# Kernel optimization log

Measured on AMD Instinct MI355X. Metric: run time of the kernel, lower is better.

The kernel has to match this reference:

```python
import jax, jax.numpy as jnp
import numpy as np

B = 65536      # total rows = env_batch(8192) * n_slave(8)
DIN = 256      # input_shape
H = 64         # slave_hidden_dim
A = 32         # attention_dim
NACT = 14      # n_actions
NS = 8         # n_slave


def setup_inputs() -> dict:
    key = jax.random.key(0)
    ks = jax.random.split(key, 12)
    s = 0.05
    return {
        "obs": jax.random.normal(ks[0], (B, DIN), jnp.float32),
        "hidden_state": jax.random.normal(ks[1], (B, H), jnp.float32),
        "enc_W": jax.random.normal(ks[2], (DIN, H), jnp.float32) * s,
        "enc_b": jnp.zeros((H,), jnp.float32),
        "gru_Wih": jax.random.normal(ks[3], (3 * H, H), jnp.float32) * s,
        "gru_Whh": jax.random.normal(ks[4], (3 * H, H), jnp.float32) * s,
        "gru_bih": jnp.zeros((3 * H,), jnp.float32),
        "gru_bhh": jnp.zeros((3 * H,), jnp.float32),
        "qW": jax.random.normal(ks[5], (H, A), jnp.float32) * s,
        "kW": jax.random.normal(ks[6], (H, A), jnp.float32) * s,
        "vW": jax.random.normal(ks[7], (H, A), jnp.float32) * s,
        "vb": jnp.zeros((A,), jnp.float32),
        "decW": jax.random.normal(ks[8], (H + A, NACT), jnp.float32) * s,
        "decb": jnp.zeros((NACT,), jnp.float32),
        "n_slave": NS,
    }


def reference(obs, hidden_state, enc_W, enc_b, gru_Wih, gru_Whh, gru_bih, gru_bhh,
              qW, kW, vW, vb, decW, decb, n_slave):
    # encoding + ReLU
    x = jax.nn.relu(obs @ enc_W + enc_b)                      # [B, H]
    # torch GRUCell: r,z,n gate order in weight rows
    gx = x @ gru_Wih.T + gru_bih                              # [B, 3H]
    gh = hidden_state @ gru_Whh.T + gru_bhh                   # [B, 3H]
    xr, xz, xn = jnp.split(gx, 3, axis=-1)
    hr, hz, hn = jnp.split(gh, 3, axis=-1)
    r = jax.nn.sigmoid(xr + hr)
    z = jax.nn.sigmoid(xz + hz)
    n = jnp.tanh(xn + r * hn)
    h_out = (1.0 - z) * n + z * hidden_state                  # [B, H]

    Ad = qW.shape[-1]
    q = (h_out @ qW).reshape(-1, n_slave, Ad)                 # [b, n, A]
    k = (h_out @ kW).reshape(-1, n_slave, Ad)
    v = jax.nn.relu(h_out @ vW + vb).reshape(-1, n_slave, Ad)

    # exclude-self attention == diagonal-masked softmax attention
    scores = jnp.einsum('bia,bja->bij', q, k) / jnp.sqrt(jnp.float32(Ad))
    eye = jnp.eye(n_slave, dtype=bool)
    scores = jnp.where(eye, jnp.float32(-1e9), scores)
    attn = jax.nn.softmax(scores, axis=-1)                    # [b, n, n]
    xatt = jnp.einsum('bij,bja->bia', attn, v).reshape(-1, Ad)  # [B, A]

    out = jnp.concatenate([h_out, xatt], axis=-1) @ decW + decb  # [B, n_actions]
    return (out, h_out)
```

## Files before the change

kernel.cpp:

```cpp
#include <hip/hip_runtime.h>


#define NACT 14
#define BTOT 65536

typedef unsigned int  u32;
typedef unsigned short u16;
using short8 = __attribute__((ext_vector_type(8))) short;
using f32x4  = __attribute__((ext_vector_type(4))) float;

#define ENCB 0
#define WIHB 16896
#define WHHB 30720
#define QKVB 44544
#define DECB 51456
#define WTOT 53120

__device__ u16   g_wbuf[WTOT];
__device__ float g_bias[256];

__device__ __forceinline__ u32 f2bf(float f){
  u32 x = __float_as_uint(f);
  return (x + 0x7fffu + ((x >> 16) & 1u)) >> 16;
}
__device__ __forceinline__ u32 pk2(float a, float b){ return f2bf(a) | (f2bf(b) << 16); }
__device__ __forceinline__ float sigm(float x){ return 1.0f / (1.0f + __expf(-x)); }
__device__ __forceinline__ float tanhp(float x){ return 1.0f - 2.0f / (__expf(2.0f * x) + 1.0f); }
__device__ __forceinline__ short8 as_s8(uint4 v){ union { uint4 u; short8 s; } x; x.u = v; return x.s; }

#define MFMA16(a,b,c) __builtin_amdgcn_mfma_f32_16x16x32_bf16((a),(b),(c),0,0,0)

__global__ void prep(const float* __restrict__ encW, const float* __restrict__ Wih,
                     const float* __restrict__ Whh,  const float* __restrict__ qW,
                     const float* __restrict__ kW,   const float* __restrict__ vW,
                     const float* __restrict__ decW, const float* __restrict__ bih,
                     const float* __restrict__ bhh)
{
  int i = blockIdx.x * 256 + threadIdx.x;
  if (blockIdx.x == 0) {
    int n = threadIdx.x & 63, g = threadIdx.x >> 6;
    float v;
    if      (g == 0) v = bih[n]       + bhh[n];
    else if (g == 1) v = bih[64 + n]  + bhh[64 + n];
    else if (g == 2) v = bih[128 + n];
    else             v = bhh[128 + n];
    g_bias[threadIdx.x] = v;
  }
  if (i >= WTOT) return;
  float val = 0.f;
  if (i < WIHB)      { int n = i / 264, k = i % 264;            if (k < 256) val = encW[k * 64 + n]; }
  else if (i < WHHB) { int j = i - WIHB; int n = j / 72, k = j % 72; if (k < 64) val = Wih[n * 64 + k]; }
  else if (i < QKVB) { int j = i - WHHB; int n = j / 72, k = j % 72; if (k < 64) val = Whh[n * 64 + k]; }
  else if (i < DECB) { int j = i - QKVB; int n = j / 72, k = j % 72;
    if (k < 64) { int m = n >> 5, nn = n & 31;
      val = (m == 0) ? qW[k * 32 + nn] * 0.17677669529663687f
          : (m == 1) ? kW[k * 32 + nn] : vW[k * 32 + nn]; } }
  else { int j = i - DECB; int n = j / 104, k = j % 104; if (n < 14 && k < 96) val = decW[k * 14 + n]; }
  g_wbuf[i] = (u16)f2bf(val);
}

__global__ __launch_bounds__(256, 3)
void commslave_main(const float* __restrict__ obs,  const float* __restrict__ hid,
                    const float* __restrict__ encb, const float* __restrict__ vb,
                    const float* __restrict__ decb, float* __restrict__ out)
{
  __shared__ __align__(16) u16 ldsU[23040];

  const int tid  = threadIdx.x;
  const int lane = tid & 63;
  const int w    = tid >> 6;
  const int quad = lane >> 4;
  const int l16  = lane & 15;
  const int M0   = 16 * w;
  const int gr   = blockIdx.x * 64 + M0;

  float* Sf = (float*)(ldsU + 9216) + w * (16 * 68);
  float* Af = (float*)(ldsU + 9216) + w * (16 * 108);

  f32x4 ce[4];
  #pragma unroll
  for (int t = 0; t < 4; t++) { float bv = encb[16 * t + l16]; ce[t] = (f32x4){bv, bv, bv, bv}; }
  #pragma unroll
  for (int ks = 0; ks < 8; ks++) {
    const float* ap = obs + (size_t)(gr + l16) * 256 + ks * 32 + quad * 8;
    float4 a0 = *(const float4*)ap, a1 = *(const float4*)(ap + 4);
    short8 a = as_s8(make_uint4(pk2(a0.x, a0.y), pk2(a0.z, a0.w), pk2(a1.x, a1.y), pk2(a1.z, a1.w)));
    #pragma unroll
    for (int t = 0; t < 4; t++) {
      short8 b = as_s8(*(const uint4*)&g_wbuf[ENCB + (16 * t + l16) * 264 + ks * 32 + quad * 8]);
      ce[t] = MFMA16(a, b, ce[t]);
    }
  }
  #pragma unroll
  for (int t = 0; t < 4; t++)
    #pragma unroll
    for (int r = 0; r < 4; r++)
      Sf[(quad * 4 + r) * 68 + 16 * t + l16] = fmaxf(ce[t][r], 0.f);
  #pragma unroll
  for (int i = 0; i < 2; i++) {
    int c = lane + 64 * i, lr = c >> 3, j = c & 7;
    const float* sp = &Sf[lr * 68 + 8 * j];
    float4 v0 = *(const float4*)sp, v1 = *(const float4*)(sp + 4);
    *(uint4*)&ldsU[(M0 + lr) * 72 + 8 * j] =
        make_uint4(pk2(v0.x, v0.y), pk2(v0.z, v0.w), pk2(v1.x, v1.y), pk2(v1.z, v1.w));
  }
  __syncthreads();

  short8 ax[2], ah[2];
  #pragma unroll
  for (int ks = 0; ks < 2; ks++) {
    ax[ks] = *(const short8*)&ldsU[(M0 + l16) * 72 + ks * 32 + quad * 8];
    const float* hp = hid + (size_t)(gr + l16) * 64 + ks * 32 + quad * 8;
    float4 h0 = *(const float4*)hp, h1 = *(const float4*)(hp + 4);
    ah[ks] = as_s8(make_uint4(pk2(h0.x, h0.y), pk2(h0.z, h0.w), pk2(h1.x, h1.y), pk2(h1.z, h1.w)));
  }
  #pragma unroll
  for (int u = 0; u < 4; u++) {
    f32x4 g6[6];
    #pragma unroll
    for (int t = 0; t < 6; t++) g6[t] = (f32x4){0.f, 0.f, 0.f, 0.f};
    #pragma unroll
    for (int g = 0; g < 3; g++) {
      int row = 64 * g + 16 * u + l16;
      #pragma unroll
      for (int ks = 0; ks < 2; ks++) {
        short8 bi = as_s8(*(const uint4*)&g_wbuf[WIHB + row * 72 + ks * 32 + quad * 8]);
        g6[g] = MFMA16(ax[ks], bi, g6[g]);
        short8 bh = as_s8(*(const uint4*)&g_wbuf[WHHB + row * 72 + ks * 32 + quad * 8]);
        g6[3 + g] = MFMA16(ah[ks], bh, g6[3 + g]);
      }
    }
    int nc = 16 * u + l16;
    float brz = g_bias[nc], bzz = g_bias[64 + nc], bni = g_bias[128 + nc], bnh = g_bias[192 + nc];
    #pragma unroll
    for (int r = 0; r < 4; r++) {
      float hp = hid[(size_t)(gr + quad * 4 + r) * 64 + nc];
      float rg = sigm(g6[0][r] + g6[3][r] + brz);
      float zg = sigm(g6[1][r] + g6[4][r] + bzz);
      float nn = tanhp(g6[2][r] + bni + rg * (g6[5][r] + bnh));
      Sf[(quad * 4 + r) * 68 + nc] = (1.f - zg) * nn + zg * hp;
    }
  }
  float* outH = out + (size_t)BTOT * NACT;
  #pragma unroll
  for (int i = 0; i < 2; i++) {
    int c = lane + 64 * i, lr = c >> 3, j = c & 7;
    const float* sp = &Sf[lr * 68 + 8 * j];
    float4 v0 = *(const float4*)sp, v1 = *(const float4*)(sp + 4);
    *(uint4*)&ldsU[4608 + (M0 + lr) * 72 + 8 * j] =
        make_uint4(pk2(v0.x, v0.y), pk2(v0.z, v0.w), pk2(v1.x, v1.y), pk2(v1.z, v1.w));
    *(float4*)(outH + (size_t)(gr + lr) * 64 + 8 * j)     = v0;
    *(float4*)(outH + (size_t)(gr + lr) * 64 + 8 * j + 4) = v1;
  }
  __syncthreads();

  short8 hx[2];
  #pragma unroll
  for (int ks = 0; ks < 2; ks++)
    hx[ks] = *(const short8*)&ldsU[4608 + (M0 + l16) * 72 + ks * 32 + quad * 8];
  f32x4 cq[6];
  #pragma unroll
  for (int t = 0; t < 6; t++) {
    float bv = (t >= 4) ? vb[16 * (t - 4) + l16] : 0.f;
    cq[t] = (f32x4){bv, bv, bv, bv};
  }
  #pragma unroll
  for (int ks = 0; ks < 2; ks++)
    #pragma unroll
    for (int t = 0; t < 6; t++) {
      short8 b = as_s8(*(const uint4*)&g_wbuf[QKVB + (16 * t + l16) * 72 + ks * 32 + quad * 8]);
      cq[t] = MFMA16(hx[ks], b, cq[t]);
    }
  #pragma unroll
  for (int t = 0; t < 6; t++)
    #pragma unroll
    for (int r = 0; r < 4; r++) {
      float v = cq[t][r];
      if (t >= 4) v = fmaxf(v, 0.f);
      Af[(quad * 4 + r) * 108 + 16 * t + l16] = v;
    }

  {
    const int r_l = lane >> 2, s4 = lane & 3;
    const int gb = r_l & 8, ri = r_l & 7;
    const float* fq = &Af[r_l * 108];
    float sc[2];
    #pragma unroll
    for (int jj = 0; jj < 2; jj++) {
      int j = s4 + 4 * jj;
      const float* fk = &Af[(gb + j) * 108 + 32];
      float d = 0.f;
      #pragma unroll
      for (int a4 = 0; a4 < 32; a4 += 4) {
        float4 q4 = *(const float4*)&fq[a4];
        float4 k4 = *(const float4*)&fk[a4];
        d += q4.x * k4.x + q4.y * k4.y + q4.z * k4.z + q4.w * k4.w;
      }
      sc[jj] = (j == ri) ? -1e30f : d;
    }
    float m = fmaxf(sc[0], sc[1]);
    m = fmaxf(m, __shfl_xor(m, 1));
    m = fmaxf(m, __shfl_xor(m, 2));
    float p0 = (s4     == ri) ? 0.f : __expf(sc[0] - m);
    float p1 = (s4 + 4 == ri) ? 0.f : __expf(sc[1] - m);
    float sum = p0 + p1;
    sum += __shfl_xor(sum, 1);
    sum += __shfl_xor(sum, 2);
    float inv = 1.f / sum;
    Af[r_l * 108 + 96 + s4]  = p0 * inv;
    Af[r_l * 108 + 100 + s4] = p1 * inv;
    float xa[8] = {0, 0, 0, 0, 0, 0, 0, 0};
    #pragma unroll
    for (int j = 0; j < 8; j++) {
      float aj = Af[r_l * 108 + 96 + j];
      const float* fv = &Af[(gb + j) * 108 + 64 + 8 * s4];
      float4 w0 = *(const float4*)fv, w1 = *(const float4*)(fv + 4);
      xa[0] += aj * w0.x; xa[1] += aj * w0.y; xa[2] += aj * w0.z; xa[3] += aj * w0.w;
      xa[4] += aj * w1.x; xa[5] += aj * w1.y; xa[6] += aj * w1.z; xa[7] += aj * w1.w;
    }
    *(uint4*)&ldsU[(M0 + r_l) * 72 + 8 * s4] =
        make_uint4(pk2(xa[0], xa[1]), pk2(xa[2], xa[3]), pk2(xa[4], xa[5]), pk2(xa[6], xa[7]));
  }
  __syncthreads();

  {
    float db = (l16 < NACT) ? decb[l16] : 0.f;
    f32x4 co = (f32x4){db, db, db, db};
    #pragma unroll
    for (int ks = 0; ks < 2; ks++) {
      short8 a = *(const short8*)&ldsU[4608 + (M0 + l16) * 72 + ks * 32 + quad * 8];
      short8 b = as_s8(*(const uint4*)&g_wbuf[DECB + l16 * 104 + ks * 32 + quad * 8]);
      co = MFMA16(a, b, co);
    }
    short8 a2 = *(const short8*)&ldsU[(M0 + l16) * 72 + quad * 8];
    short8 b2 = as_s8(*(const uint4*)&g_wbuf[DECB + l16 * 104 + 64 + quad * 8]);
    co = MFMA16(a2, b2, co);
    if (l16 < NACT) {
      #pragma unroll
      for (int r = 0; r < 4; r++)
        out[(size_t)(gr + quad * 4 + r) * NACT + l16] = co[r];
    }
  }
}

extern "C" void kernel_launch(void* const* d_in, const int* in_sizes, int n_in,
                              void* d_out, int out_size, void* d_ws, size_t ws_size,
                              hipStream_t stream) {
  (void)in_sizes; (void)n_in; (void)d_ws; (void)ws_size; (void)out_size;
  const float* obs  = (const float*)d_in[0];
  const float* hid  = (const float*)d_in[1];
  const float* encW = (const float*)d_in[2];
  const float* encb = (const float*)d_in[3];
  const float* Wih  = (const float*)d_in[4];
  const float* Whh  = (const float*)d_in[5];
  const float* bih  = (const float*)d_in[6];
  const float* bhh  = (const float*)d_in[7];
  const float* qW   = (const float*)d_in[8];
  const float* kW   = (const float*)d_in[9];
  const float* vW   = (const float*)d_in[10];
  const float* vb   = (const float*)d_in[11];
  const float* decW = (const float*)d_in[12];
  const float* decb = (const float*)d_in[13];
  float* out = (float*)d_out;

  prep<<<(WTOT + 255) / 256, 256, 0, stream>>>(encW, Wih, Whh, qW, kW, vW, decW, bih, bhh);
  commslave_main<<<BTOT / 64, 256, 0, stream>>>(obs, hid, encb, vb, decb, out);
}
```

Measured before the change: 163.3 us.

## Shrink blocks, stage hidden state in LDS as bf16, use hardware bf16 pack

Blocks drop from 256 to 128 threads and LDS from 46KB to about 18KB to raise occupancy. The hidden state is loaded once with coalesced reads, stored in LDS as bf16, and reused for the GRU MFMA operand and the blend term instead of being read from global memory twice. V is kept in bf16 LDS and the f32 attention buffer is merged with the scratch area. h_out is written to global memory at the end from its bf16 copy, and float-to-bf16 packing now uses the v_cvt_pk_bf16_f32 instruction. The cost is lower precision: the hidden-state blend term and the h_out output are now rounded to bf16.

```diff
diff --git a/kernel.cpp b/kernel.cpp
--- a/kernel.cpp
+++ b/kernel.cpp
@@ -19,11 +19,17 @@
 __device__ u16   g_wbuf[WTOT];
 __device__ float g_bias[256];
 
-__device__ __forceinline__ u32 f2bf(float f){
+__device__ __forceinline__ u32 f2bf_rne(float f){
   u32 x = __float_as_uint(f);
   return (x + 0x7fffu + ((x >> 16) & 1u)) >> 16;
 }
-__device__ __forceinline__ u32 pk2(float a, float b){ return f2bf(a) | (f2bf(b) << 16); }
+__device__ __forceinline__ u32 pk2(float a, float b){
+  u32 d;
+  asm("v_cvt_pk_bf16_f32 %0, %1, %2" : "=v"(d) : "v"(a), "v"(b));
+  return d;
+}
+__device__ __forceinline__ float blo(u32 u){ return __uint_as_float(u << 16); }
+__device__ __forceinline__ float bhi(u32 u){ return __uint_as_float(u & 0xffff0000u); }
 __device__ __forceinline__ float sigm(float x){ return 1.0f / (1.0f + __expf(-x)); }
 __device__ __forceinline__ float tanhp(float x){ return 1.0f - 2.0f / (__expf(2.0f * x) + 1.0f); }
 __device__ __forceinline__ short8 as_s8(uint4 v){ union { uint4 u; short8 s; } x; x.u = v; return x.s; }
@@ -56,15 +62,15 @@
       val = (m == 0) ? qW[k * 32 + nn] * 0.17677669529663687f
           : (m == 1) ? kW[k * 32 + nn] : vW[k * 32 + nn]; } }
   else { int j = i - DECB; int n = j / 104, k = j % 104; if (n < 14 && k < 96) val = decW[k * 14 + n]; }
-  g_wbuf[i] = (u16)f2bf(val);
-}
-
-__global__ __launch_bounds__(256, 3)
+  g_wbuf[i] = (u16)f2bf_rne(val);
+}
+
+__global__ __launch_bounds__(128, 4)
 void commslave_main(const float* __restrict__ obs,  const float* __restrict__ hid,
                     const float* __restrict__ encb, const float* __restrict__ vb,
                     const float* __restrict__ decb, float* __restrict__ out)
 {
-  __shared__ __align__(16) u16 ldsU[23040];
+  __shared__ __align__(16) u16 ldsU[8960];
 
   const int tid  = threadIdx.x;
   const int lane = tid & 63;
@@ -72,10 +78,16 @@
   const int quad = lane >> 4;
   const int l16  = lane & 15;
   const int M0   = 16 * w;
-  const int gr   = blockIdx.x * 64 + M0;
-
-  float* Sf = (float*)(ldsU + 9216) + w * (16 * 68);
-  float* Af = (float*)(ldsU + 9216) + w * (16 * 108);
+  const int gr   = blockIdx.x * 32 + M0;
+  float* Sf = (float*)(ldsU + 4608) + w * (16 * 68);
+
+  #pragma unroll
+  for (int i = 0; i < 4; i++) {
+    int c = lane + 64 * i;
+    int lr = c >> 4, c4 = c & 15;
+    float4 v = ((const float4*)hid)[(size_t)(gr + lr) * 16 + c4];
+    *(uint2*)&ldsU[2304 + (M0 + lr) * 72 + c4 * 4] = make_uint2(pk2(v.x, v.y), pk2(v.z, v.w));
+  }
 
   f32x4 ce[4];
   #pragma unroll
@@ -110,9 +122,7 @@
   #pragma unroll
   for (int ks = 0; ks < 2; ks++) {
     ax[ks] = *(const short8*)&ldsU[(M0 + l16) * 72 + ks * 32 + quad * 8];
-    const float* hp = hid + (size_t)(gr + l16) * 64 + ks * 32 + quad * 8;
-    float4 h0 = *(const float4*)hp, h1 = *(const float4*)(hp + 4);
-    ah[ks] = as_s8(make_uint4(pk2(h0.x, h0.y), pk2(h0.z, h0.w), pk2(h1.x, h1.y), pk2(h1.z, h1.w)));
+    ah[ks] = *(const short8*)&ldsU[2304 + (M0 + l16) * 72 + ks * 32 + quad * 8];
   }
   #pragma unroll
   for (int u = 0; u < 4; u++) {
@@ -134,30 +144,27 @@
     float brz = g_bias[nc], bzz = g_bias[64 + nc], bni = g_bias[128 + nc], bnh = g_bias[192 + nc];
     #pragma unroll
     for (int r = 0; r < 4; r++) {
-      float hp = hid[(size_t)(gr + quad * 4 + r) * 64 + nc];
+      float hp = blo(ldsU[2304 + (M0 + quad * 4 + r) * 72 + nc]);
       float rg = sigm(g6[0][r] + g6[3][r] + brz);
       float zg = sigm(g6[1][r] + g6[4][r] + bzz);
       float nn = tanhp(g6[2][r] + bni + rg * (g6[5][r] + bnh));
       Sf[(quad * 4 + r) * 68 + nc] = (1.f - zg) * nn + zg * hp;
     }
   }
-  float* outH = out + (size_t)BTOT * NACT;
   #pragma unroll
   for (int i = 0; i < 2; i++) {
     int c = lane + 64 * i, lr = c >> 3, j = c & 7;
     const float* sp = &Sf[lr * 68 + 8 * j];
     float4 v0 = *(const float4*)sp, v1 = *(const float4*)(sp + 4);
-    *(uint4*)&ldsU[4608 + (M0 + lr) * 72 + 8 * j] =
+    *(uint4*)&ldsU[2304 + (M0 + lr) * 72 + 8 * j] =
         make_uint4(pk2(v0.x, v0.y), pk2(v0.z, v0.w), pk2(v1.x, v1.y), pk2(v1.z, v1.w));
-    *(float4*)(outH + (size_t)(gr + lr) * 64 + 8 * j)     = v0;
-    *(float4*)(outH + (size_t)(gr + lr) * 64 + 8 * j + 4) = v1;
   }
   __syncthreads();
 
   short8 hx[2];
   #pragma unroll
   for (int ks = 0; ks < 2; ks++)
-    hx[ks] = *(const short8*)&ldsU[4608 + (M0 + l16) * 72 + ks * 32 + quad * 8];
+    hx[ks] = *(const short8*)&ldsU[2304 + (M0 + l16) * 72 + ks * 32 + quad * 8];
   f32x4 cq[6];
   #pragma unroll
   for (int t = 0; t < 6; t++) {
@@ -172,23 +179,27 @@
       cq[t] = MFMA16(hx[ks], b, cq[t]);
     }
   #pragma unroll
-  for (int t = 0; t < 6; t++)
-    #pragma unroll
-    for (int r = 0; r < 4; r++) {
-      float v = cq[t][r];
-      if (t >= 4) v = fmaxf(v, 0.f);
-      Af[(quad * 4 + r) * 108 + 16 * t + l16] = v;
-    }
+  for (int t = 0; t < 4; t++)
+    #pragma unroll
+    for (int r = 0; r < 4; r++)
+      Sf[(quad * 4 + r) * 68 + 16 * t + l16] = cq[t][r];
+  #pragma unroll
+  for (int t = 4; t < 6; t++)
+    #pragma unroll
+    for (int r = 0; r < 4; r++)
+      ldsU[(M0 + quad * 4 + r) * 72 + 32 + 16 * (t - 4) + l16] =
+          (u16)pk2(fmaxf(cq[t][r], 0.f), 0.f);
+  __syncthreads();
 
   {
     const int r_l = lane >> 2, s4 = lane & 3;
     const int gb = r_l & 8, ri = r_l & 7;
-    const float* fq = &Af[r_l * 108];
+    const float* fq = &Sf[r_l * 68];
     float sc[2];
     #pragma unroll
     for (int jj = 0; jj < 2; jj++) {
       int j = s4 + 4 * jj;
-      const float* fk = &Af[(gb + j) * 108 + 32];
+      const float* fk = &Sf[(gb + j) * 68 + 32];
       float d = 0.f;
       #pragma unroll
       for (int a4 = 0; a4 < 32; a4 += 4) {
@@ -207,16 +218,17 @@
     sum += __shfl_xor(sum, 1);
     sum += __shfl_xor(sum, 2);
     float inv = 1.f / sum;
-    Af[r_l * 108 + 96 + s4]  = p0 * inv;
-    Af[r_l * 108 + 100 + s4] = p1 * inv;
+    Sf[r_l * 68 + s4]     = p0 * inv;
+    Sf[r_l * 68 + 4 + s4] = p1 * inv;
     float xa[8] = {0, 0, 0, 0, 0, 0, 0, 0};
     #pragma unroll
     for (int j = 0; j < 8; j++) {
-      float aj = Af[r_l * 108 + 96 + j];
-      const float* fv = &Af[(gb + j) * 108 + 64 + 8 * s4];
-      float4 w0 = *(const float4*)fv, w1 = *(const float4*)(fv + 4);
-      xa[0] += aj * w0.x; xa[1] += aj * w0.y; xa[2] += aj * w0.z; xa[3] += aj * w0.w;
-      xa[4] += aj * w1.x; xa[5] += aj * w1.y; xa[6] += aj * w1.z; xa[7] += aj * w1.w;
+      float aj = Sf[r_l * 68 + j];
+      uint4 uv = *(const uint4*)&ldsU[(M0 + gb + j) * 72 + 32 + 8 * s4];
+      xa[0] += aj * blo(uv.x); xa[1] += aj * bhi(uv.x);
+      xa[2] += aj * blo(uv.y); xa[3] += aj * bhi(uv.y);
+      xa[4] += aj * blo(uv.z); xa[5] += aj * bhi(uv.z);
+      xa[6] += aj * blo(uv.w); xa[7] += aj * bhi(uv.w);
     }
     *(uint4*)&ldsU[(M0 + r_l) * 72 + 8 * s4] =
         make_uint4(pk2(xa[0], xa[1]), pk2(xa[2], xa[3]), pk2(xa[4], xa[5]), pk2(xa[6], xa[7]));
@@ -228,7 +240,7 @@
     f32x4 co = (f32x4){db, db, db, db};
     #pragma unroll
     for (int ks = 0; ks < 2; ks++) {
-      short8 a = *(const short8*)&ldsU[4608 + (M0 + l16) * 72 + ks * 32 + quad * 8];
+      short8 a = *(const short8*)&ldsU[2304 + (M0 + l16) * 72 + ks * 32 + quad * 8];
       short8 b = as_s8(*(const uint4*)&g_wbuf[DECB + l16 * 104 + ks * 32 + quad * 8]);
       co = MFMA16(a, b, co);
     }
@@ -239,6 +251,19 @@
       #pragma unroll
       for (int r = 0; r < 4; r++)
         out[(size_t)(gr + quad * 4 + r) * NACT + l16] = co[r];
+    }
+  }
+
+  {
+    float* outH = out + (size_t)BTOT * NACT;
+    #pragma unroll
+    for (int i = 0; i < 2; i++) {
+      int c = lane + 64 * i, lr = c >> 3, j = c & 7;
+      uint4 u = *(const uint4*)&ldsU[2304 + (M0 + lr) * 72 + 8 * j];
+      *(float4*)(outH + (size_t)(gr + lr) * 64 + 8 * j) =
+          make_float4(blo(u.x), bhi(u.x), blo(u.y), bhi(u.y));
+      *(float4*)(outH + (size_t)(gr + lr) * 64 + 8 * j + 4) =
+          make_float4(blo(u.z), bhi(u.z), blo(u.w), bhi(u.w));
     }
   }
 }
@@ -264,5 +289,5 @@
   float* out = (float*)d_out;
 
   prep<<<(WTOT + 255) / 256, 256, 0, stream>>>(encW, Wih, Whh, qW, kW, vW, decW, bih, bhh);
-  commslave_main<<<BTOT / 64, 256, 0, stream>>>(obs, hid, encb, vb, decb, out);
-}
+  commslave_main<<<BTOT / 32, 128, 0, stream>>>(obs, hid, encb, vb, decb, out);
+}
```

New measurement: 163.7 us. About the same (+0.2%).
